# Kernel tuning notes

Measured on AMD Instinct MI355X. Metric: run time of the kernel, lower is better.

## Reference

```python
import jax, jax.numpy as jnp
import numpy as np

SIZE = 512
CHUNK = 16
NEG = -1e30  # stands in for -inf z key of invalid pixels
W_ATOL = 1e-8  # torch.isclose(w, 0) default atol


def setup_inputs() -> dict:
    key = jax.random.key(0)
    tris = jax.random.normal(key, (512, 3, 3), dtype=jnp.float32)  # [T,3,3] verts xyz in view space
    return {"tris": tris}


def _area2d(a, b, c):
    # (b.x - a.x)*(c.y - a.y) - (b.y - a.y)*(c.x - a.x); `a` may be batched [..., 2]
    return (b[0] - a[..., 0]) * (c[1] - a[..., 1]) - (b[1] - a[..., 1]) * (c[0] - a[..., 0])


def _tri_key_pts(tri, pts, xi, yi):
    """Per-triangle z key ([H,W], NEG where not covered) and interpolated 3d pts [H,W,3]."""
    t2 = tri[:, :2]
    w = _area2d(t2[0], t2[1], t2[2])  # signed parallelogram area, scalar
    pAB = _area2d(pts, t2[0], t2[1])
    pBC = _area2d(pts, t2[1], t2[2])
    pCA = _area2d(pts, t2[2], t2[0])
    inside = (pAB > 0) & (pBC > 0) & (pCA > 0)  # inside_mask: all sub-areas strictly positive
    # aabb clamped to [-1,1], converted to pixel indices with truncation (box2pts semantics)
    lo = jnp.clip(jnp.min(t2, axis=0), -1.0, 1.0)
    hi = jnp.clip(jnp.max(t2, axis=0), -1.0, 1.0)
    bb = ((jnp.concatenate([lo, hi]) + 1.0) * 0.5 * SIZE).astype(jnp.int32)
    inbox = (xi >= bb[0]) & (xi < bb[2]) & (yi >= bb[1]) & (yi < bb[3])
    valid_w = jnp.abs(w) > W_ATOL  # skip degenerate tri (torch.isclose(w, 0))
    sw = jnp.where(valid_w, w, 1.0)
    w1 = pAB / sw
    w2 = pBC / sw
    w3 = 1.0 - w1 - w2
    p3 = w1[..., None] * tri[0] + w2[..., None] * tri[1] + w3[..., None] * tri[2]  # [H,W,3]
    valid = inside & inbox & valid_w
    keyz = jnp.where(valid, p3[..., 2], jnp.asarray(NEG, p3.dtype))
    return keyz, p3


def _render(tris):
    T = tris.shape[0]
    lin = jnp.linspace(-1.0, 1.0, SIZE, dtype=tris.dtype)
    px, py = jnp.meshgrid(lin, lin, indexing="ij")  # lookup_table
    pts = jnp.stack([px, py], axis=-1)  # [H,W,2]
    xi, yi = jnp.meshgrid(jnp.arange(SIZE), jnp.arange(SIZE), indexing="ij")
    zmin = jnp.min(tris[..., 2])  # initial zbuffer value
    tris_c = tris.reshape(T // CHUNK, CHUNK, 3, 3)

    def step(carry, tchunk):
        zbuf, res = carry
        keyz, p3 = jax.vmap(_tri_key_pts, in_axes=(0, None, None, None))(tchunk, pts, xi, yi)
        idx = CHUNK - 1 - jnp.argmax(keyz[::-1], axis=0)  # last argmax in chunk
        bz = jnp.take_along_axis(keyz, idx[None], axis=0)[0]  # [H,W]
        bp = jnp.take_along_axis(p3, idx[None, ..., None], axis=0)[0]  # [H,W,3]
        upd = bz >= zbuf  # invalid pixels carry NEG and never pass
        zbuf = jnp.where(upd, bz, zbuf)
        new = jnp.concatenate([bp, jnp.ones_like(bp[..., :1])], axis=-1)  # rgb=pts3d, alpha=1
        res = jnp.where(upd[..., None], new, res)
        return (zbuf, res), None

    init = (jnp.full((SIZE, SIZE), zmin, dtype=tris.dtype), jnp.zeros((SIZE, SIZE, 4), dtype=tris.dtype))
    (zbuf, res), _ = jax.lax.scan(jax.checkpoint(step), init, tris_c)
    return res


def reference(tris):
    return _render(tris)
```

## Files before the change

### kernel.cpp

```cpp
#include <hip/hip_runtime.h>

#define SIZE 512
#define NTRI 512

#pragma clang fp contract(off)

__device__ __forceinline__ float lin_at(int i) {
    if (i == SIZE - 1) return 1.0f;
    float s = __fdiv_rn((float)i, 511.0f);
    float u = 1.0f - s;
    return s - u;
}

__device__ __forceinline__ float4 shade(const float* __restrict__ tris, int bi,
                                        float px, float py) {
#pragma clang fp contract(off)
    if (bi < 0) return make_float4(0.0f, 0.0f, 0.0f, 0.0f);
    const float* p = tris + bi * 9;
    float a0 = p[0], a1 = p[1], a2 = p[2];
    float b0 = p[3], b1 = p[4], b2 = p[5];
    float c0 = p[6], c1 = p[7], c2 = p[8];
    float w = (b0 - a0) * (c1 - a1) - (b1 - a1) * (c0 - a0);
    float sw = (fabsf(w) > 1e-8f) ? w : 1.0f;
    float dax = a0 - px, day = a1 - py;
    float dbx = b0 - px, dby = b1 - py;
    float dcx = c0 - px, dcy = c1 - py;
    float pAB = dax * dby - day * dbx;
    float pBC = dbx * dcy - dby * dcx;
    float w1 = __fdiv_rn(pAB, sw);
    float w2 = __fdiv_rn(pBC, sw);
    float w3 = 1.0f - w1 - w2;
    float x = (w1 * a0 + w2 * b0) + w3 * c0;
    float y = (w1 * a1 + w2 * b1) + w3 * c1;
    float z = (w1 * a2 + w2 * b2) + w3 * c2;
    return make_float4(x, y, z, 1.0f);
}

__global__ __launch_bounds__(512, 8) void render_kernel(const float* __restrict__ tris,
                                                        float* __restrict__ out) {
#pragma clang fp contract(off)
    __shared__ float4 szp[NTRI];
    __shared__ int4   sbb[NTRI];
    __shared__ float4 sv0[NTRI];
    __shared__ float2 sv1[NTRI];
    __shared__ unsigned long long smA[8], smB[8], smC[8];
    __shared__ float sredz[8], sredm[8];
    __shared__ float2 smrg[256];

    const int tid = threadIdx.x;
    const int lane = tid & 63, wv = tid >> 6;
    const unsigned long long lt = (1ull << lane) - 1ull;

    const int i0 = blockIdx.y * 16;
    const int j0 = blockIdx.x * 16;

    const float pxlo = lin_at(i0), pxhi = lin_at(i0 + 15);
    const float pylo = lin_at(j0), pyhi = lin_at(j0 + 15);

    const int t = tid;
    const float* p = tris + t * 9;
    float a0 = p[0], a1 = p[1], a2 = p[2];
    float b0 = p[3], b1 = p[4], b2 = p[5];
    float c0 = p[6], c1 = p[7], c2 = p[8];

    float zm = fminf(a2, fminf(b2, c2));

    float w = (b0 - a0) * (c1 - a1) - (b1 - a1) * (c0 - a0);
    bool vw = fabsf(w) > 1e-8f;
    float sw = vw ? w : 1.0f;

    float lox = fminf(fminf(a0, b0), c0);
    float loy = fminf(fminf(a1, b1), c1);
    float hix = fmaxf(fmaxf(a0, b0), c0);
    float hiy = fmaxf(fmaxf(a1, b1), c1);
    int bb0 = (int)((fminf(fmaxf(lox, -1.0f), 1.0f) + 1.0f) * 0.5f * 512.0f);
    int bb1 = (int)((fminf(fmaxf(loy, -1.0f), 1.0f) + 1.0f) * 0.5f * 512.0f);
    int bb2 = (int)((fminf(fmaxf(hix, -1.0f), 1.0f) + 1.0f) * 0.5f * 512.0f);
    int bb3 = (int)((fminf(fmaxf(hiy, -1.0f), 1.0f) + 1.0f) * 0.5f * 512.0f);

    bool cand = vw && (w > -1e-4f) &&
                (bb0 < i0 + 16) && (bb2 > i0) &&
                (bb1 < j0 + 16) && (bb3 > j0);

    float cAB = a0 * b1 - a1 * b0, gxAB = a1 - b1, gyAB = b0 - a0;
    float cBC = b0 * c1 - b1 * c0, gxBC = b1 - c1, gyBC = c0 - b0;
    float cCA = c0 * a1 - c1 * a0, gxCA = c1 - a1, gyCA = a0 - c0;

    bool allIn = false;
    if (cand) {
        float x0, x1, y0, y1, mx, mn;
        x0 = gxAB * pxlo; x1 = gxAB * pxhi; y0 = gyAB * pylo; y1 = gyAB * pyhi;
        mx = cAB + fmaxf(x0, x1) + fmaxf(y0, y1);
        mn = cAB + fminf(x0, x1) + fminf(y0, y1);
        cand = mx >= -1e-3f;
        allIn = mn > 1e-3f;
        x0 = gxBC * pxlo; x1 = gxBC * pxhi; y0 = gyBC * pylo; y1 = gyBC * pyhi;
        mx = cBC + fmaxf(x0, x1) + fmaxf(y0, y1);
        mn = cBC + fminf(x0, x1) + fminf(y0, y1);
        cand = cand && (mx >= -1e-3f);
        allIn = allIn && (mn > 1e-3f);
        x0 = gxCA * pxlo; x1 = gxCA * pxhi; y0 = gyCA * pylo; y1 = gyCA * pyhi;
        mx = cCA + fmaxf(x0, x1) + fmaxf(y0, y1);
        mn = cCA + fminf(x0, x1) + fminf(y0, y1);
        cand = cand && (mx >= -1e-3f);
        allIn = allIn && (mn > 1e-3f);
    }

    float rsw = __builtin_amdgcn_rcpf(sw);
    float k1 = (a2 - c2) * rsw;
    float k2 = (b2 - c2) * rsw;
    float zc = c2 + k1 * cAB + k2 * cBC;
    float zx = k1 * gxAB + k2 * gxBC;
    float zy = k1 * gyAB + k2 * gyBC;

    float zxl = zx * pxlo, zxh = zx * pxhi;
    float zyl = zy * pylo, zyh = zy * pyhi;
    float tzmin = zc + fminf(zxl, zxh) + fminf(zyl, zyh);
    float tzmax = zc + fmaxf(zxl, zxh) + fmaxf(zyl, zyh);

    bool full = (bb0 <= i0) && (bb2 >= i0 + 16) &&
                (bb1 <= j0) && (bb3 >= j0 + 16);
    bool vIF = cand && allIn && full;
    bool vIP = cand && allIn && !full;
    bool vEX = cand && !allIn;

    float mloc = vIF ? tzmin : -1e30f;

    for (int off = 32; off; off >>= 1) {
        zm = fminf(zm, __shfl_xor(zm, off));
        mloc = fmaxf(mloc, __shfl_xor(mloc, off));
    }
    if (lane == 0) { sredz[wv] = zm; sredm[wv] = mloc; }
    __syncthreads();
    float zmin = sredz[0], M = sredm[0];
#pragma unroll
    for (int g = 1; g < 8; ++g) { zmin = fminf(zmin, sredz[g]); M = fmaxf(M, sredm[g]); }
    const float cullb = fmaxf(M, zmin) - 1e-4f;

    {
        bool keep = tzmax >= cullb;
        vIF &= keep; vIP &= keep; vEX &= keep;
        unsigned long long mA = __ballot(vIF);
        unsigned long long mB = __ballot(vIP);
        unsigned long long mC = __ballot(vEX);
        if (lane == 0) { smA[wv] = mA; smB[wv] = mB; smC[wv] = mC; }
    }
    __syncthreads();

    int bA[8], bB[8], bC[8], c = 0;
#pragma unroll
    for (int g = 0; g < 8; ++g) { bA[g] = c; c += __popcll(smA[g]); }
    const int cntA = c;
#pragma unroll
    for (int g = 0; g < 8; ++g) { bB[g] = c; c += __popcll(smB[g]); }
    const int cntB = c;
#pragma unroll
    for (int g = 0; g < 8; ++g) { bC[g] = c; c += __popcll(smC[g]); }
    const int cntC = c;

    if (vIF || vIP || vEX) {
        int pos;
        if (vIF)      pos = bA[wv] + __popcll(smA[wv] & lt);
        else if (vIP) pos = bB[wv] + __popcll(smB[wv] & lt);
        else          pos = bC[wv] + __popcll(smC[wv] & lt);

        szp[pos] = make_float4(zc, zx, zy, __int_as_float(t));
        if (!vIF) sbb[pos] = make_int4(bb0, bb1, bb2, bb3);
        if (vEX) {
            sv0[pos] = make_float4(a0, a1, b0, b1);
            sv1[pos] = make_float2(c0, c1);
        }
    }
    __syncthreads();

    const int pix = tid & 255;
    const int h   = tid >> 8;
    const int tx  = pix & 15;
    const int tyq = pix >> 4;
    const int j = j0 + tx;
    const int i = i0 + tyq;
    const float px = lin_at(i);
    const float py = lin_at(j);

    float best = zmin;
    int   bt = -1;

#pragma unroll 4
    for (int k = h; k < cntA; k += 2) {
        float4 zp = szp[k];
        float z = fmaf(zp.y, px, fmaf(zp.z, py, zp.x));
        if (z >= best) { best = z; bt = __float_as_int(zp.w); }
    }
#pragma unroll 4
    for (int k = cntA + h; k < cntB; k += 2) {
        float4 zp = szp[k];
        int4 bb = sbb[k];
        float z = fmaf(zp.y, px, fmaf(zp.z, py, zp.x));
        bool in = (i >= bb.x) & (i < bb.z) & (j >= bb.y) & (j < bb.w);
        if (in & (z >= best)) { best = z; bt = __float_as_int(zp.w); }
    }
#pragma unroll 2
    for (int k = cntB + h; k < cntC; k += 2) {
        float4 zp = szp[k];
        float4 f0 = sv0[k];
        float2 f1 = sv1[k];
        int4 bb = sbb[k];
        float dax = f0.x - px, day = f0.y - py;
        float dbx = f0.z - px, dby = f0.w - py;
        float dcx = f1.x - px, dcy = f1.y - py;
        float pAB = dax * dby - day * dbx;
        float pBC = dbx * dcy - dby * dcx;
        float pCA = dcx * day - dcy * dax;
        bool cov = (pAB > 0.0f) & (pBC > 0.0f) & (pCA > 0.0f) &
                   (i >= bb.x) & (i < bb.z) & (j >= bb.y) & (j < bb.w);
        float z = fmaf(zp.y, px, fmaf(zp.z, py, zp.x));
        if (cov & (z >= best)) { best = z; bt = __float_as_int(zp.w); }
    }

    if (h == 1) smrg[pix] = make_float2(best, __int_as_float(bt));
    __syncthreads();
    if (h == 0) {
        float2 o = smrg[pix];
        float zB = o.x;
        int tB = __float_as_int(o.y);
        if ((zB > best) | ((zB == best) & (tB > bt))) { best = zB; bt = tB; }
        ((float4*)out)[i * SIZE + j] = shade(tris, bt, px, py);
    }
}

extern "C" void kernel_launch(void* const* d_in, const int* in_sizes, int n_in,
                              void* d_out, int out_size, void* d_ws, size_t ws_size,
                              hipStream_t stream) {
    const float* tris = (const float*)d_in[0];
    float* out = (float*)d_out;
    dim3 grid(SIZE / 16, SIZE / 16, 1);
    dim3 block(512, 1, 1);
    render_kernel<<<grid, block, 0, stream>>>(tris, out);
}
```

Measured before the change: 15.20 us.

## Use 32x32 tiles with two pixels per thread and stage triangles in LDS

Each block now covers a 32x32 pixel tile instead of 16x16, so it launches 256 blocks instead of 1024. Each thread evaluates two pixel rows per candidate triangle instead of splitting the triangle list across two half-blocks, which removes the cross-half merge and its barrier. All triangle data is first copied into shared memory, so per-triangle setup, edge tests and final shading read from LDS rather than global memory. The per-block culling setup is paid less often, but each tile has more candidate triangles, and the smaller grid may underfill the GPU's many compute units.

New measurement: 12.48 us. 1.22x faster.

```diff
diff --git a/kernel.cpp b/kernel.cpp
--- a/kernel.cpp
+++ b/kernel.cpp
@@ -12,11 +12,11 @@
     return s - u;
 }
 
-__device__ __forceinline__ float4 shade(const float* __restrict__ tris, int bi,
-                                        float px, float py) {
+__device__ __forceinline__ float4 shade_lds(const float* __restrict__ st, int bi,
+                                            float px, float py) {
 #pragma clang fp contract(off)
     if (bi < 0) return make_float4(0.0f, 0.0f, 0.0f, 0.0f);
-    const float* p = tris + bi * 9;
+    const float* p = st + bi * 9;
     float a0 = p[0], a1 = p[1], a2 = p[2];
     float b0 = p[3], b1 = p[4], b2 = p[5];
     float c0 = p[6], c1 = p[7], c2 = p[8];
@@ -36,29 +36,34 @@
     return make_float4(x, y, z, 1.0f);
 }
 
-__global__ __launch_bounds__(512, 8) void render_kernel(const float* __restrict__ tris,
-                                                        float* __restrict__ out) {
+__global__ __launch_bounds__(512) void render_kernel(const float* __restrict__ tris,
+                                                     float* __restrict__ out) {
 #pragma clang fp contract(off)
+    __shared__ float  stris[NTRI * 9];
     __shared__ float4 szp[NTRI];
     __shared__ int4   sbb[NTRI];
-    __shared__ float4 sv0[NTRI];
-    __shared__ float2 sv1[NTRI];
     __shared__ unsigned long long smA[8], smB[8], smC[8];
     __shared__ float sredz[8], sredm[8];
-    __shared__ float2 smrg[256];
 
     const int tid = threadIdx.x;
     const int lane = tid & 63, wv = tid >> 6;
     const unsigned long long lt = (1ull << lane) - 1ull;
 
-    const int i0 = blockIdx.y * 16;
-    const int j0 = blockIdx.x * 16;
-
-    const float pxlo = lin_at(i0), pxhi = lin_at(i0 + 15);
-    const float pylo = lin_at(j0), pyhi = lin_at(j0 + 15);
+    const int i0 = blockIdx.y * 32;
+    const int j0 = blockIdx.x * 32;
+
+    const float pxlo = lin_at(i0), pxhi = lin_at(i0 + 31);
+    const float pylo = lin_at(j0), pyhi = lin_at(j0 + 31);
+
+    {
+        const float4* g4 = (const float4*)tris;
+        float4* s4 = (float4*)stris;
+        for (int k = tid; k < NTRI * 9 / 4; k += 512) s4[k] = g4[k];
+    }
+    __syncthreads();
 
     const int t = tid;
-    const float* p = tris + t * 9;
+    const float* p = &stris[t * 9];
     float a0 = p[0], a1 = p[1], a2 = p[2];
     float b0 = p[3], b1 = p[4], b2 = p[5];
     float c0 = p[6], c1 = p[7], c2 = p[8];
@@ -79,8 +84,8 @@
     int bb3 = (int)((fminf(fmaxf(hiy, -1.0f), 1.0f) + 1.0f) * 0.5f * 512.0f);
 
     bool cand = vw && (w > -1e-4f) &&
-                (bb0 < i0 + 16) && (bb2 > i0) &&
-                (bb1 < j0 + 16) && (bb3 > j0);
+                (bb0 < i0 + 32) && (bb2 > i0) &&
+                (bb1 < j0 + 32) && (bb3 > j0);
 
     float cAB = a0 * b1 - a1 * b0, gxAB = a1 - b1, gyAB = b0 - a0;
     float cBC = b0 * c1 - b1 * c0, gxBC = b1 - c1, gyBC = c0 - b0;
@@ -118,8 +123,8 @@
     float tzmin = zc + fminf(zxl, zxh) + fminf(zyl, zyh);
     float tzmax = zc + fmaxf(zxl, zxh) + fmaxf(zyl, zyh);
 
-    bool full = (bb0 <= i0) && (bb2 >= i0 + 16) &&
-                (bb1 <= j0) && (bb3 >= j0 + 16);
+    bool full = (bb0 <= i0) && (bb2 >= i0 + 32) &&
+                (bb1 <= j0) && (bb3 >= j0 + 32);
     bool vIF = cand && allIn && full;
     bool vIP = cand && allIn && !full;
     bool vEX = cand && !allIn;
@@ -166,66 +171,79 @@
 
         szp[pos] = make_float4(zc, zx, zy, __int_as_float(t));
         if (!vIF) sbb[pos] = make_int4(bb0, bb1, bb2, bb3);
-        if (vEX) {
-            sv0[pos] = make_float4(a0, a1, b0, b1);
-            sv1[pos] = make_float2(c0, c1);
-        }
-    }
-    __syncthreads();
-
-    const int pix = tid & 255;
-    const int h   = tid >> 8;
-    const int tx  = pix & 15;
-    const int tyq = pix >> 4;
-    const int j = j0 + tx;
-    const int i = i0 + tyq;
-    const float px = lin_at(i);
-    const float py = lin_at(j);
-
-    float best = zmin;
-    int   bt = -1;
+    }
+    __syncthreads();
+
+    const int tx  = tid & 31;
+    const int tyq = tid >> 5;
+    const int j  = j0 + tx;
+    const int iA = i0 + tyq;
+    const int iB = iA + 16;
+    const float pxA = lin_at(iA);
+    const float pxB = lin_at(iB);
+    const float py  = lin_at(j);
+
+    float bestA = zmin, bestB = zmin;
+    int   btA = -1,     btB = -1;
 
 #pragma unroll 4
-    for (int k = h; k < cntA; k += 2) {
+    for (int k = 0; k < cntA; ++k) {
         float4 zp = szp[k];
-        float z = fmaf(zp.y, px, fmaf(zp.z, py, zp.x));
-        if (z >= best) { best = z; bt = __float_as_int(zp.w); }
+        float base = fmaf(zp.z, py, zp.x);
+        float zA = fmaf(zp.y, pxA, base);
+        float zB = fmaf(zp.y, pxB, base);
+        if (zA >= bestA) { bestA = zA; btA = __float_as_int(zp.w); }
+        if (zB >= bestB) { bestB = zB; btB = __float_as_int(zp.w); }
     }
 #pragma unroll 4
-    for (int k = cntA + h; k < cntB; k += 2) {
+    for (int k = cntA; k < cntB; ++k) {
         float4 zp = szp[k];
         int4 bb = sbb[k];
-        float z = fmaf(zp.y, px, fmaf(zp.z, py, zp.x));
-        bool in = (i >= bb.x) & (i < bb.z) & (j >= bb.y) & (j < bb.w);
-        if (in & (z >= best)) { best = z; bt = __float_as_int(zp.w); }
+        float base = fmaf(zp.z, py, zp.x);
+        float zA = fmaf(zp.y, pxA, base);
+        float zB = fmaf(zp.y, pxB, base);
+        bool inJ = (j >= bb.y) & (j < bb.w);
+        bool inA = (iA >= bb.x) & (iA < bb.z) & inJ;
+        bool inB = (iB >= bb.x) & (iB < bb.z) & inJ;
+        if (inA & (zA >= bestA)) { bestA = zA; btA = __float_as_int(zp.w); }
+        if (inB & (zB >= bestB)) { bestB = zB; btB = __float_as_int(zp.w); }
     }
 #pragma unroll 2
-    for (int k = cntB + h; k < cntC; k += 2) {
+    for (int k = cntB; k < cntC; ++k) {
         float4 zp = szp[k];
-        float4 f0 = sv0[k];
-        float2 f1 = sv1[k];
         int4 bb = sbb[k];
-        float dax = f0.x - px, day = f0.y - py;
-        float dbx = f0.z - px, dby = f0.w - py;
-        float dcx = f1.x - px, dcy = f1.y - py;
-        float pAB = dax * dby - day * dbx;
-        float pBC = dbx * dcy - dby * dcx;
-        float pCA = dcx * day - dcy * dax;
-        bool cov = (pAB > 0.0f) & (pBC > 0.0f) & (pCA > 0.0f) &
-                   (i >= bb.x) & (i < bb.z) & (j >= bb.y) & (j < bb.w);
-        float z = fmaf(zp.y, px, fmaf(zp.z, py, zp.x));
-        if (cov & (z >= best)) { best = z; bt = __float_as_int(zp.w); }
-    }
-
-    if (h == 1) smrg[pix] = make_float2(best, __int_as_float(bt));
-    __syncthreads();
-    if (h == 0) {
-        float2 o = smrg[pix];
-        float zB = o.x;
-        int tB = __float_as_int(o.y);
-        if ((zB > best) | ((zB == best) & (tB > bt))) { best = zB; bt = tB; }
-        ((float4*)out)[i * SIZE + j] = shade(tris, bt, px, py);
-    }
+        const int tt = __float_as_int(zp.w);
+        const float* q = &stris[tt * 9];
+        float qa0 = q[0], qa1 = q[1];
+        float qb0 = q[3], qb1 = q[4];
+        float qc0 = q[6], qc1 = q[7];
+        float day = qa1 - py, dby = qb1 - py, dcy = qc1 - py;
+        float base = fmaf(zp.z, py, zp.x);
+        bool inJ = (j >= bb.y) & (j < bb.w);
+        {
+            float dax = qa0 - pxA, dbx = qb0 - pxA, dcx = qc0 - pxA;
+            float pAB = dax * dby - day * dbx;
+            float pBC = dbx * dcy - dby * dcx;
+            float pCA = dcx * day - dcy * dax;
+            bool cov = (pAB > 0.0f) & (pBC > 0.0f) & (pCA > 0.0f) &
+                       (iA >= bb.x) & (iA < bb.z) & inJ;
+            float zA = fmaf(zp.y, pxA, base);
+            if (cov & (zA >= bestA)) { bestA = zA; btA = tt; }
+        }
+        {
+            float dax = qa0 - pxB, dbx = qb0 - pxB, dcx = qc0 - pxB;
+            float pAB = dax * dby - day * dbx;
+            float pBC = dbx * dcy - dby * dcx;
+            float pCA = dcx * day - dcy * dax;
+            bool cov = (pAB > 0.0f) & (pBC > 0.0f) & (pCA > 0.0f) &
+                       (iB >= bb.x) & (iB < bb.z) & inJ;
+            float zB = fmaf(zp.y, pxB, base);
+            if (cov & (zB >= bestB)) { bestB = zB; btB = tt; }
+        }
+    }
+
+    ((float4*)out)[iA * SIZE + j] = shade_lds(stris, btA, pxA, py);
+    ((float4*)out)[iB * SIZE + j] = shade_lds(stris, btB, pxB, py);
 }
 
 extern "C" void kernel_launch(void* const* d_in, const int* in_sizes, int n_in,
@@ -233,7 +251,7 @@
                               hipStream_t stream) {
     const float* tris = (const float*)d_in[0];
     float* out = (float*)d_out;
-    dim3 grid(SIZE / 16, SIZE / 16, 1);
+    dim3 grid(SIZE / 32, SIZE / 32, 1);
     dim3 block(512, 1, 1);
     render_kernel<<<grid, block, 0, stream>>>(tris, out);
 }
```
